# Kernel tuning notes

Measured on AMD Instinct MI355X. Metric: run time of the kernel, lower is better.

The kernel has to match this reference:

```python
import jax, jax.numpy as jnp
import numpy as np

NUM_CLASSES = 50000
NUM_SAMPLED = 1000
D_MODEL = 1024
BATCH, SEQ = 32, 512


def _log_expected_count(ids, num_sampled, num_classes):
    # TF log-uniform candidate sampler (unique=True):
    # P(c) = log((c+2)/(c+1)) / log(num_classes+1)
    # E[count] = -expm1(num_sampled * log1p(-P))
    ids_f = ids.astype(jnp.float32)
    p = (jnp.log(ids_f + 2.0) - jnp.log(ids_f + 1.0)) / np.float32(np.log(num_classes + 1.0))
    return jnp.log(-jnp.expm1(num_sampled * jnp.log1p(-p)))


def setup_inputs() -> dict:
    key = jax.random.key(0)
    k1, k2, k3, k4 = jax.random.split(key, 4)
    lstm_outputs = jax.random.normal(k1, (BATCH, SEQ, D_MODEL), dtype=jnp.float32)
    next_token_ids = jax.random.randint(k2, (BATCH, SEQ), 0, NUM_CLASSES)
    sampled_ids = jax.random.randint(k3, (BATCH, NUM_SAMPLED), 0, NUM_CLASSES)
    W = jax.random.normal(k4, (NUM_CLASSES, D_MODEL), dtype=jnp.float32) * (1.0 / np.sqrt(D_MODEL))
    b = jnp.zeros((NUM_CLASSES,), dtype=jnp.float32)
    return {"lstm_outputs": lstm_outputs, "next_token_ids": next_token_ids,
            "sampled_ids": sampled_ids, "W": W, "b": b}


def reference(lstm_outputs, next_token_ids, sampled_ids, W, b):
    # Vectorized sampled-softmax loss (tf.nn.sampled_softmax_loss with
    # log-uniform sampler, partition_strategy irrelevant, accidental-hit removal),
    # mapped over the batch dim as the original tf.map_fn does.
    log_q_true = _log_expected_count(next_token_ids, NUM_SAMPLED, NUM_CLASSES)   # [B,T]
    log_q_samp = _log_expected_count(sampled_ids, NUM_SAMPLED, NUM_CLASSES)      # [B,S]

    w_true = W[next_token_ids]                                                   # [B,T,D]
    true_logit = (jnp.einsum('btd,btd->bt', lstm_outputs, w_true)
                  + b[next_token_ids] - log_q_true)                              # [B,T]

    w_samp = W[sampled_ids]                                                      # [B,S,D]
    samp_logits = (jnp.einsum('btd,bsd->bts', lstm_outputs, w_samp)
                   + b[sampled_ids][:, None, :] - log_q_samp[:, None, :])        # [B,T,S]

    # remove accidental hits (sampled id == true label)
    hit = sampled_ids[:, None, :] == next_token_ids[:, :, None]                  # [B,T,S]
    samp_logits = jnp.where(hit, jnp.float32(-1e9), samp_logits)

    all_logits = jnp.concatenate([true_logit[..., None], samp_logits], axis=-1)  # [B,T,1+S]
    # softmax CE with true class at index 0
    losses = jax.nn.logsumexp(all_logits, axis=-1) - true_logit                  # [B,T]
    return 0.5 * jnp.mean(losses)
```

## Files before the change

### kernel.cpp

```cpp
#include <hip/hip_runtime.h>
#include <cmath>

#define BATCH 32
#define SEQLEN 512
#define NSAMP 1000
#define DMODEL 1024
#define NCHUNK 4

typedef __bf16 bf16x8_t __attribute__((ext_vector_type(8)));
typedef float f32x4_t __attribute__((ext_vector_type(4)));

__device__ __forceinline__ unsigned pack_bf2(float lo, float hi) {
    unsigned ulo = __float_as_uint(lo);
    unsigned uhi = __float_as_uint(hi);
    ulo = (ulo + 0x7fffu + ((ulo >> 16) & 1u)) >> 16;
    uhi = (uhi + 0x7fffu + ((uhi >> 16) & 1u)) & 0xffff0000u;
    return (ulo & 0xffffu) | uhi;
}

__device__ __forceinline__ float log_expected_count(int id) {
    float idf = (float)id;
    float p = log1pf(1.0f / (idf + 1.0f)) * 0.09242316f;
    return logf(-expm1f(1000.0f * log1pf(-p)));
}

__device__ __forceinline__ void gl16(const void* g, void* l) {
    __builtin_amdgcn_global_load_lds(
        (const __attribute__((address_space(1))) unsigned int*)g,
        (__attribute__((address_space(3))) unsigned int*)l,
        16, 0, 0);
}

__global__ __launch_bounds__(256) void prep_kernel(
    const float* __restrict__ h, const int* __restrict__ labels,
    const int* __restrict__ sids, const float* __restrict__ W,
    const float* __restrict__ bias, unsigned short* __restrict__ Wb,
    unsigned short* __restrict__ hb,
    float* __restrict__ adjw, float* __restrict__ tlw)
{
    const int w = threadIdx.x >> 6, lane = threadIdx.x & 63;
    if (blockIdx.x < 8000) {
        const int row = blockIdx.x * 4 + w;
        const int sv = sids[row];
        const float4* src = (const float4*)(W + (size_t)sv * DMODEL);
        unsigned short* dst = Wb + (size_t)row * DMODEL;
#pragma unroll
        for (int j = 0; j < 4; ++j) {
            float4 v = src[lane + j * 64];
            uint2 u;
            u.x = pack_bf2(v.x, v.y);
            u.y = pack_bf2(v.z, v.w);
            *(uint2*)(dst + (lane + j * 64) * 4) = u;
        }
        if (lane == 0) adjw[row] = bias[sv] - log_expected_count(sv);
    } else {
        const int r = (blockIdx.x - 8000) * 4 + w;
        const int lab = labels[r];
        const float4* hp = (const float4*)(h + (size_t)r * DMODEL);
        const float4* wp = (const float4*)(W + (size_t)lab * DMODEL);
        unsigned short* hdst = hb + (size_t)r * DMODEL;
        float s = 0.0f;
#pragma unroll
        for (int j = 0; j < 4; ++j) {
            float4 a = hp[lane + j * 64];
            float4 c = wp[lane + j * 64];
            s += a.x * c.x + a.y * c.y + a.z * c.z + a.w * c.w;
            uint2 u;
            u.x = pack_bf2(a.x, a.y);
            u.y = pack_bf2(a.z, a.w);
            *(uint2*)(hdst + (lane + j * 64) * 4) = u;
        }
#pragma unroll
        for (int off = 32; off > 0; off >>= 1) s += __shfl_xor(s, off, 64);
        if (lane == 0) tlw[r] = s + bias[lab] - log_expected_count(lab);
    }
}

__global__ __launch_bounds__(512, 2) void sampled_softmax_main(
    const int* __restrict__ labels, const int* __restrict__ sids,
    const unsigned short* __restrict__ hb, const unsigned short* __restrict__ Wb,
    const float* __restrict__ adjw,
    float* __restrict__ pm, float* __restrict__ pl)
{
    __shared__ __align__(16) unsigned short Ab[3][256 * 32];
    __shared__ __align__(16) unsigned short Bb[3][256 * 32];
    __shared__ int   sid_lds[256];
    __shared__ float adj_lds[256];
    __shared__ int   lab_lds[256];
    __shared__ float mpart[4][256];
    __shared__ float lpart[4][256];

    const int wg     = blockIdx.x;
    const int bb     = wg & 31;
    const int rest   = wg >> 5;
    const int tile_t = rest & 1;
    const int chunk  = rest >> 1;
    const int t0  = tile_t * 256;
    const int tid = threadIdx.x;
    const int wv  = tid >> 6, l = tid & 63;
    const int wr  = wv >> 2, wc = wv & 3;
    const int lm  = l & 15,  q = l >> 4;
    const int rl4 = l >> 2,  cp = l & 3;

    if (tid < 256) {
        const int s = chunk * 256 + tid;
        const bool v = s < NSAMP;
        sid_lds[tid] = v ? sids[bb * NSAMP + s] : -1;
        adj_lds[tid] = v ? adjw[bb * NSAMP + s] : 0.0f;
        lab_lds[tid] = labels[bb * SEQLEN + t0 + tid];
    }

    const int swzs = (rl4 & 3) ^ ((rl4 >> 2) & 3);
    const int cs = (cp ^ swzs) * 8;
    const unsigned short* aS0 = hb + (size_t)(bb * SEQLEN + t0 + 32 * wv + rl4) * DMODEL + cs;
    const unsigned short* aS1 = aS0 + (size_t)16 * DMODEL;
    int rb0 = chunk * 256 + 32 * wv + rl4;
    int rb1 = rb0 + 16;
    if (rb0 > NSAMP - 1) rb0 = NSAMP - 1;
    if (rb1 > NSAMP - 1) rb1 = NSAMP - 1;
    const unsigned short* bS0 = Wb + (size_t)(bb * NSAMP + rb0) * DMODEL + cs;
    const unsigned short* bS1 = Wb + (size_t)(bb * NSAMP + rb1) * DMODEL + cs;

#define STAGE_TILE(KT, BUF)                                                   \
    do {                                                                      \
        const int _adv = (KT) * 32;                                           \
        gl16(aS0 + _adv, &Ab[BUF][(32 * wv) * 32]);                           \
        gl16(aS1 + _adv, &Ab[BUF][(32 * wv + 16) * 32]);                      \
        gl16(bS0 + _adv, &Bb[BUF][(32 * wv) * 32]);                           \
        gl16(bS1 + _adv, &Bb[BUF][(32 * wv + 16) * 32]);                      \
    } while (0)

    const int fswz = (lm & 3) ^ ((lm >> 2) & 3);
    const int fp = (q ^ fswz) * 8;
    int aoff[8], boff[4];
#pragma unroll
    for (int t = 0; t < 8; ++t) aoff[t] = (128 * wr + 16 * t + lm) * 32 + fp;
#pragma unroll
    for (int c = 0; c < 4; ++c) boff[c] = (64 * wc + 16 * c + lm) * 32 + fp;

    f32x4_t acc[8][4];
#pragma unroll
    for (int t = 0; t < 8; ++t)
#pragma unroll
        for (int c = 0; c < 4; ++c) acc[t][c] = (f32x4_t){0.f, 0.f, 0.f, 0.f};

    STAGE_TILE(0, 0);
    STAGE_TILE(1, 1);
    asm volatile("s_waitcnt lgkmcnt(0)" ::: "memory");
    __builtin_amdgcn_s_barrier();

#pragma unroll
    for (int kt = 0; kt < 32; ++kt) {
        if (kt < 31) { asm volatile("s_waitcnt vmcnt(4)" ::: "memory"); }
        else         { asm volatile("s_waitcnt vmcnt(0)" ::: "memory"); }
        __builtin_amdgcn_s_barrier();
        if (kt + 2 < 32) STAGE_TILE(kt + 2, (kt + 2) % 3);

        const unsigned short* Ac = Ab[kt % 3];
        const unsigned short* Bc = Bb[kt % 3];
        bf16x8_t fa[8];
#pragma unroll
        for (int t = 0; t < 8; ++t) fa[t] = *(const bf16x8_t*)(Ac + aoff[t]);
        __builtin_amdgcn_s_setprio(1);
#pragma unroll
        for (int c = 0; c < 4; ++c) {
            bf16x8_t fb = *(const bf16x8_t*)(Bc + boff[c]);
#pragma unroll
            for (int t = 0; t < 8; ++t)
                acc[t][c] = __builtin_amdgcn_mfma_f32_16x16x32_bf16(fa[t], fb, acc[t][c], 0, 0, 0);
        }
        __builtin_amdgcn_s_setprio(0);
    }
#undef STAGE_TILE

    float adjv[4]; int sidv[4]; bool cval[4];
#pragma unroll
    for (int c = 0; c < 4; ++c) {
        const int col = 64 * wc + 16 * c + lm;
        adjv[c] = adj_lds[col];
        sidv[c] = sid_lds[col];
        cval[c] = (chunk * 256 + col) < NSAMP;
    }
#pragma unroll
    for (int t = 0; t < 8; ++t) {
#pragma unroll
        for (int i = 0; i < 4; ++i) {
            const int r = 128 * wr + 16 * t + 4 * q + i;
            const int lab = lab_lds[r];
            float x[4]; bool ok[4];
            float m = -INFINITY;
#pragma unroll
            for (int c = 0; c < 4; ++c) {
                x[c] = acc[t][c][i] + adjv[c];
                ok[c] = cval[c] && (sidv[c] != lab);
                if (ok[c]) m = fmaxf(m, x[c]);
            }
            float ls = 0.0f;
#pragma unroll
            for (int c = 0; c < 4; ++c) ls += ok[c] ? __expf(x[c] - m) : 0.0f;
#pragma unroll
            for (int off = 1; off < 16; off <<= 1) {
                const float mo = __shfl_xor(m, off, 64);
                const float lo = __shfl_xor(ls, off, 64);
                const float M  = fmaxf(m, mo);
                const float e1 = (ls > 0.0f) ? ls * __expf(m - M) : 0.0f;
                const float e2 = (lo > 0.0f) ? lo * __expf(mo - M) : 0.0f;
                m = M; ls = e1 + e2;
            }
            if (lm == 0) { mpart[wc][r] = m; lpart[wc][r] = ls; }
        }
    }
    __syncthreads();
    if (tid < 256) {
        float m = -INFINITY, lsum = 0.0f;
#pragma unroll
        for (int p = 0; p < 4; ++p) {
            const float mp = mpart[p][tid];
            const float lp = lpart[p][tid];
            if (lp > 0.0f) {
                if (mp > m) { lsum = lsum * __expf(m - mp) + lp; m = mp; }
                else        { lsum += lp * __expf(mp - m); }
            }
        }
        const int idx = (bb * SEQLEN + t0 + tid) * NCHUNK + chunk;
        pm[idx] = m;
        pl[idx] = lsum;
    }
}

__global__ __launch_bounds__(256) void combine_kernel(
    const float* __restrict__ pm, const float* __restrict__ pl,
    const float* __restrict__ tlw, float* __restrict__ bsum)
{
    __shared__ float wsum[4];
    const int tid = threadIdx.x;
    const int w = tid >> 6, lane = tid & 63;
    const int idx = blockIdx.x * 256 + tid;
    float m = -INFINITY, l = 0.0f;
#pragma unroll
    for (int c = 0; c < NCHUNK; ++c) {
        const float mp = pm[idx * NCHUNK + c];
        const float lp = pl[idx * NCHUNK + c];
        if (lp > 0.0f) {
            if (mp > m) { l = l * __expf(m - mp) + lp; m = mp; }
            else        { l += lp * __expf(mp - m); }
        }
    }
    const float t = tlw[idx];
    const float M = fmaxf(m, t);
    float loss = __logf(l * __expf(m - M) + __expf(t - M)) + M - t;
#pragma unroll
    for (int off = 32; off > 0; off >>= 1) loss += __shfl_xor(loss, off, 64);
    if (lane == 0) wsum[w] = loss;
    __syncthreads();
    if (tid == 0) bsum[blockIdx.x] = wsum[0] + wsum[1] + wsum[2] + wsum[3];
}

__global__ void finalize_kernel(const float* __restrict__ bsum, float* __restrict__ out) {
    float v = bsum[threadIdx.x];
#pragma unroll
    for (int off = 32; off > 0; off >>= 1) v += __shfl_xor(v, off, 64);
    if (threadIdx.x == 0) out[0] = v * (0.5f / (float)(BATCH * SEQLEN));
}

extern "C" void kernel_launch(void* const* d_in, const int* in_sizes, int n_in,
                              void* d_out, int out_size, void* d_ws, size_t ws_size,
                              hipStream_t stream) {
    const float* h      = (const float*)d_in[0];
    const int*   labels = (const int*)d_in[1];
    const int*   sids   = (const int*)d_in[2];
    const float* W      = (const float*)d_in[3];
    const float* bias   = (const float*)d_in[4];

    char* base = (char*)d_ws;
    unsigned short* Wb = (unsigned short*)base;
    unsigned short* hb = (unsigned short*)(base + 65536000);
    float* adjw = (float*)(base + 99090432);
    float* tlw  = (float*)(base + 99218432);
    float* pmw  = (float*)(base + 99283968);
    float* plw  = (float*)(base + 99546112);
    float* bsum = (float*)(base + 99808256);

    prep_kernel<<<dim3(12096), dim3(256), 0, stream>>>(h, labels, sids, W, bias, Wb, hb, adjw, tlw);
    sampled_softmax_main<<<dim3(256), dim3(512), 0, stream>>>(
        labels, sids, hb, Wb, adjw, pmw, plw);
    combine_kernel<<<dim3(64), dim3(256), 0, stream>>>(pmw, plw, tlw, bsum);
    finalize_kernel<<<dim3(1), dim3(64), 0, stream>>>(bsum, (float*)d_out);
}
```

Baseline: 394.8 us.

## Double K-tile depth to 64 with double-buffered LDS and 8-way swizzle

The GEMM main loop now stages 64-wide K tiles instead of 32, halving the number of loop iterations, and each tile is consumed in two MFMA sub-steps. LDS buffering goes from triple to double, and the swizzle is redone over 8 chunks to fit the wider rows. The next tile is now loaded into the just-freed buffer after the compute, behind an extra barrier. The aim is fewer waits per unit of K and wider global loads. In exchange LDS use grows and the prefetch is issued later in each iteration, which may expose more load latency.

```diff
diff --git a/kernel.cpp b/kernel.cpp
--- a/kernel.cpp
+++ b/kernel.cpp
@@ -82,8 +82,8 @@
     const float* __restrict__ adjw,
     float* __restrict__ pm, float* __restrict__ pl)
 {
-    __shared__ __align__(16) unsigned short Ab[3][256 * 32];
-    __shared__ __align__(16) unsigned short Bb[3][256 * 32];
+    __shared__ __align__(16) unsigned short Ab[2][256 * 64];
+    __shared__ __align__(16) unsigned short Bb[2][256 * 64];
     __shared__ int   sid_lds[256];
     __shared__ float adj_lds[256];
     __shared__ int   lab_lds[256];
@@ -100,7 +100,7 @@
     const int wv  = tid >> 6, l = tid & 63;
     const int wr  = wv >> 2, wc = wv & 3;
     const int lm  = l & 15,  q = l >> 4;
-    const int rl4 = l >> 2,  cp = l & 3;
+    const int rl8 = l >> 3,  cp8 = l & 7;
 
     if (tid < 256) {
         const int s = chunk * 256 + tid;
@@ -110,33 +110,36 @@
         lab_lds[tid] = labels[bb * SEQLEN + t0 + tid];
     }
 
-    const int swzs = (rl4 & 3) ^ ((rl4 >> 2) & 3);
-    const int cs = (cp ^ swzs) * 8;
-    const unsigned short* aS0 = hb + (size_t)(bb * SEQLEN + t0 + 32 * wv + rl4) * DMODEL + cs;
-    const unsigned short* aS1 = aS0 + (size_t)16 * DMODEL;
-    int rb0 = chunk * 256 + 32 * wv + rl4;
-    int rb1 = rb0 + 16;
-    if (rb0 > NSAMP - 1) rb0 = NSAMP - 1;
-    if (rb1 > NSAMP - 1) rb1 = NSAMP - 1;
-    const unsigned short* bS0 = Wb + (size_t)(bb * NSAMP + rb0) * DMODEL + cs;
-    const unsigned short* bS1 = Wb + (size_t)(bb * NSAMP + rb1) * DMODEL + cs;
+    const int csg = (cp8 ^ rl8) * 8;
+    const unsigned short* aSrc = hb + (size_t)(bb * SEQLEN + t0 + 32 * wv + rl8) * DMODEL + csg;
+    const unsigned short* bSrc[4];
+#pragma unroll
+    for (int j = 0; j < 4; ++j) {
+        int rb = chunk * 256 + 32 * wv + 8 * j + rl8;
+        if (rb > NSAMP - 1) rb = NSAMP - 1;
+        bSrc[j] = Wb + (size_t)(bb * NSAMP + rb) * DMODEL + csg;
+    }
 
 #define STAGE_TILE(KT, BUF)                                                   \
     do {                                                                      \
-        const int _adv = (KT) * 32;                                           \
-        gl16(aS0 + _adv, &Ab[BUF][(32 * wv) * 32]);                           \
-        gl16(aS1 + _adv, &Ab[BUF][(32 * wv + 16) * 32]);                      \
-        gl16(bS0 + _adv, &Bb[BUF][(32 * wv) * 32]);                           \
-        gl16(bS1 + _adv, &Bb[BUF][(32 * wv + 16) * 32]);                      \
+        const size_t _adv = (size_t)(KT) * 64;                                \
+        gl16(aSrc + _adv,                 &Ab[BUF][(32 * wv     ) * 64]);     \
+        gl16(aSrc + 8 * DMODEL + _adv,    &Ab[BUF][(32 * wv +  8) * 64]);     \
+        gl16(aSrc + 16 * DMODEL + _adv,   &Ab[BUF][(32 * wv + 16) * 64]);     \
+        gl16(aSrc + 24 * DMODEL + _adv,   &Ab[BUF][(32 * wv + 24) * 64]);     \
+        gl16(bSrc[0] + _adv, &Bb[BUF][(32 * wv     ) * 64]);                  \
+        gl16(bSrc[1] + _adv, &Bb[BUF][(32 * wv +  8) * 64]);                  \
+        gl16(bSrc[2] + _adv, &Bb[BUF][(32 * wv + 16) * 64]);                  \
+        gl16(bSrc[3] + _adv, &Bb[BUF][(32 * wv + 24) * 64]);                  \
     } while (0)
 
-    const int fswz = (lm & 3) ^ ((lm >> 2) & 3);
-    const int fp = (q ^ fswz) * 8;
-    int aoff[8], boff[4];
-#pragma unroll
-    for (int t = 0; t < 8; ++t) aoff[t] = (128 * wr + 16 * t + lm) * 32 + fp;
-#pragma unroll
-    for (int c = 0; c < 4; ++c) boff[c] = (64 * wc + 16 * c + lm) * 32 + fp;
+    const int ck0 = ((0 + q) ^ (lm & 7)) * 8;
+    const int ck1 = ((4 + q) ^ (lm & 7)) * 8;
+    int rowA[8], rowB[4];
+#pragma unroll
+    for (int t = 0; t < 8; ++t) rowA[t] = (128 * wr + 16 * t + lm) * 64;
+#pragma unroll
+    for (int c = 0; c < 4; ++c) rowB[c] = (64 * wc + 16 * c + lm) * 64;
 
     f32x4_t acc[8][4];
 #pragma unroll
@@ -150,26 +153,34 @@
     __builtin_amdgcn_s_barrier();
 
 #pragma unroll
-    for (int kt = 0; kt < 32; ++kt) {
-        if (kt < 31) { asm volatile("s_waitcnt vmcnt(4)" ::: "memory"); }
+    for (int kt = 0; kt < 16; ++kt) {
+        if (kt < 15) { asm volatile("s_waitcnt vmcnt(8)" ::: "memory"); }
         else         { asm volatile("s_waitcnt vmcnt(0)" ::: "memory"); }
         __builtin_amdgcn_s_barrier();
-        if (kt + 2 < 32) STAGE_TILE(kt + 2, (kt + 2) % 3);
-
-        const unsigned short* Ac = Ab[kt % 3];
-        const unsigned short* Bc = Bb[kt % 3];
-        bf16x8_t fa[8];
-#pragma unroll
-        for (int t = 0; t < 8; ++t) fa[t] = *(const bf16x8_t*)(Ac + aoff[t]);
-        __builtin_amdgcn_s_setprio(1);
-#pragma unroll
-        for (int c = 0; c < 4; ++c) {
-            bf16x8_t fb = *(const bf16x8_t*)(Bc + boff[c]);
-#pragma unroll
-            for (int t = 0; t < 8; ++t)
-                acc[t][c] = __builtin_amdgcn_mfma_f32_16x16x32_bf16(fa[t], fb, acc[t][c], 0, 0, 0);
-        }
-        __builtin_amdgcn_s_setprio(0);
+
+        const unsigned short* Ac = Ab[kt & 1];
+        const unsigned short* Bc = Bb[kt & 1];
+#pragma unroll
+        for (int s = 0; s < 2; ++s) {
+            const int ck = s ? ck1 : ck0;
+            bf16x8_t fa[8];
+#pragma unroll
+            for (int t = 0; t < 8; ++t) fa[t] = *(const bf16x8_t*)(Ac + rowA[t] + ck);
+            __builtin_amdgcn_s_setprio(1);
+#pragma unroll
+            for (int c = 0; c < 4; ++c) {
+                bf16x8_t fb = *(const bf16x8_t*)(Bc + rowB[c] + ck);
+#pragma unroll
+                for (int t = 0; t < 8; ++t)
+                    acc[t][c] = __builtin_amdgcn_mfma_f32_16x16x32_bf16(fa[t], fb, acc[t][c], 0, 0, 0);
+            }
+            __builtin_amdgcn_s_setprio(0);
+        }
+
+        if (kt + 2 < 16) {
+            __builtin_amdgcn_s_barrier();
+            STAGE_TILE(kt + 2, kt & 1);
+        }
     }
 #undef STAGE_TILE
 
```

New measurement: 384.9 us. 2.5% less time.
